# Kernel optimization log

Measured on AMD Instinct MI355X. Metric: run time of the kernel, lower is better.

The kernel has to match this reference:

```python
import jax, jax.numpy as jnp
import numpy as np


def _normal_distance(n1, n2):
    # Cosine-style normal distance: 1 - <n1, n2>. The original module stubs
    # this as 0; we use the canonical mesh-normal loss so the cdist+argmin+
    # gather chain is exercised end-to-end.
    return 1.0 - jnp.sum(n1 * n2, axis=-1)


def setup_inputs() -> dict:
    key = jax.random.key(0)
    k1, k2, k3, k4 = jax.random.split(key, 4)
    N, M = 8192, 32768
    pred_pts = jax.random.normal(k1, (1, N, 3), dtype=jnp.float32)
    pred_nrm = jax.random.normal(k2, (1, N, 3), dtype=jnp.float32)
    gt_pts = jax.random.normal(k3, (1, M, 3), dtype=jnp.float32)
    gt_nrm = jax.random.normal(k4, (1, M, 3), dtype=jnp.float32)
    # unit normals, as on a real mesh
    pred_nrm = pred_nrm / jnp.linalg.norm(pred_nrm, axis=-1, keepdims=True)
    gt_nrm = gt_nrm / jnp.linalg.norm(gt_nrm, axis=-1, keepdims=True)
    return {
        "predicted_points_batch": pred_pts,
        "predicted_normals_batch": pred_nrm,
        "gt_points_batch": gt_pts,
        "gt_normals_batch": gt_nrm,
    }


def reference(predicted_points_batch, predicted_normals_batch,
              gt_points_batch, gt_normals_batch):
    # Original forward returns inside the first loop iteration -> element 0 only.
    p = predicted_points_batch[0]    # [N,3]
    pn = predicted_normals_batch[0]  # [N,3]
    g = gt_points_batch[0]           # [M,3]
    gn = gt_normals_batch[0]         # [M,3]

    # Squared pairwise distances (monotone in true cdist; only argmin is used).
    # d2[i,j] = |p_i|^2 + |g_j|^2 - 2 p_i . g_j   -> one [N,M] intermediate.
    d2 = (jnp.sum(p * p, axis=1)[:, None]
          + jnp.sum(g * g, axis=1)[None, :]
          - 2.0 * (p @ g.T))                      # [N,M]

    gt_idx = jnp.argmin(d2, axis=1)    # nearest gt point per predicted point, [N]
    pr_idx = jnp.argmin(d2, axis=0)    # nearest predicted point per gt point, [M]

    nearest_gt_normals = gn[gt_idx]    # [N,3]
    nearest_pr_normals = pn[pr_idx]    # [M,3]

    dist1 = _normal_distance(pn, nearest_gt_normals)  # [N]
    dist2 = _normal_distance(gn, nearest_pr_normals)  # [M]
    return jnp.mean(dist1) + jnp.mean(dist2)
```

## Files before the change

kernel.cpp:

```cpp
#include <hip/hip_runtime.h>
#include <stdint.h>
#include <float.h>

#define BLK 256
#define IPT 8
#define OWNERS (BLK * IPT)
#define SLICE 128
#define SUB 64

typedef unsigned long long ull;

__device__ __forceinline__ unsigned int ford(float f) {
    int b = __float_as_int(f);
    return (b >= 0) ? ((unsigned)b ^ 0x80000000u) : ~(unsigned)b;
}
__device__ __forceinline__ float ford_inv(unsigned int u) {
    int b = (u & 0x80000000u) ? (int)(u ^ 0x80000000u) : (int)~u;
    return __int_as_float(b);
}

__global__ __launch_bounds__(BLK) void nn_min_dual(
    const float* __restrict__ p, const float* __restrict__ g,
    ull* __restrict__ rowmin, ull* __restrict__ colmin,
    int rowBlocks, int rowSlices, int colSlices)
{
    __shared__ float4 sb[SLICE];

    const float* A; const float* B; ull* outmin; int id, nSlices;
    if ((int)blockIdx.x < rowBlocks) {
        id = blockIdx.x;             A = p; B = g; outmin = rowmin; nSlices = rowSlices;
    } else {
        id = blockIdx.x - rowBlocks; A = g; B = p; outmin = colmin; nSlices = colSlices;
    }
    const int chunk = id / nSlices;
    const int slice = id - chunk * nSlices;
    const int s0 = slice * SLICE;

    if (threadIdx.x < SLICE) {
        int s = s0 + threadIdx.x;
        float bx = B[3 * s], by = B[3 * s + 1], bz = B[3 * s + 2];
        float w = fmaf(bz, bz, fmaf(by, by, bx * bx));
        sb[threadIdx.x] = make_float4(bx, by, bz, w);
    }

    const int o0 = chunk * OWNERS + threadIdx.x;
    float ax[IPT], ay[IPT], az[IPT], best[IPT];
    int base[IPT];
#pragma unroll
    for (int r = 0; r < IPT; ++r) {
        int o = o0 + r * BLK;
        ax[r] = -2.0f * A[3 * o];
        ay[r] = -2.0f * A[3 * o + 1];
        az[r] = -2.0f * A[3 * o + 2];
        best[r] = FLT_MAX;
        base[r] = s0;
    }
    __syncthreads();

    for (int st = 0; st < SLICE; st += SUB) {
        float prev[IPT];
#pragma unroll
        for (int r = 0; r < IPT; ++r) prev[r] = best[r];
#pragma unroll 4
        for (int k = st; k < st + SUB; ++k) {
            float4 q = sb[k];
#pragma unroll
            for (int r = 0; r < IPT; ++r) {
                float v = fmaf(ax[r], q.x, fmaf(ay[r], q.y, fmaf(az[r], q.z, q.w)));
                best[r] = fminf(best[r], v);
            }
        }
#pragma unroll
        for (int r = 0; r < IPT; ++r)
            if (best[r] < prev[r]) base[r] = s0 + st;
    }

#pragma unroll
    for (int r = 0; r < IPT; ++r) {
        ull packed = ((ull)ford(best[r]) << 32) | (unsigned)base[r];
        atomicMin(&outmin[o0 + r * BLK], packed);
    }
}

__global__ __launch_bounds__(BLK) void finalize_kernel(
    const ull* __restrict__ rowmin, const ull* __restrict__ colmin,
    const float* __restrict__ p, const float* __restrict__ g,
    const float* __restrict__ pn, const float* __restrict__ gn,
    float* __restrict__ out, int N, int M, float invN, float invM)
{
    int t = blockIdx.x * BLK + threadIdx.x;
    float c = 0.0f;
    if (t < N + M) {
        const float* A; const float* B; const float* An; const float* Bn;
        ull packed; int o; float inv;
        if (t < N) { o = t;     A = p; B = g; An = pn; Bn = gn; packed = rowmin[o]; inv = invN; }
        else       { o = t - N; A = g; B = p; An = gn; Bn = pn; packed = colmin[o]; inv = invM; }

        float ax = -2.0f * A[3 * o];
        float ay = -2.0f * A[3 * o + 1];
        float az = -2.0f * A[3 * o + 2];
        float bestf = ford_inv((unsigned int)(packed >> 32));
        int base = (int)(packed & 0xffffffffull);

        int idx = base;
        for (int j = 0; j < SUB; ++j) {
            int s = base + j;
            float bx = B[3 * s], by = B[3 * s + 1], bz = B[3 * s + 2];
            float w = fmaf(bz, bz, fmaf(by, by, bx * bx));
            float v = fmaf(ax, bx, fmaf(ay, by, fmaf(az, bz, w)));
            if (v == bestf) { idx = s; break; }
        }

        float d = An[3 * o] * Bn[3 * idx] + An[3 * o + 1] * Bn[3 * idx + 1]
                + An[3 * o + 2] * Bn[3 * idx + 2];
        c = (1.0f - d) * inv;
    }
#pragma unroll
    for (int off = 32; off > 0; off >>= 1) c += __shfl_down(c, off, 64);
    __shared__ float partial[BLK / 64];
    if ((threadIdx.x & 63) == 0) partial[threadIdx.x >> 6] = c;
    __syncthreads();
    if (threadIdx.x == 0) {
        float s = 0.0f;
#pragma unroll
        for (int w = 0; w < BLK / 64; ++w) s += partial[w];
        atomicAdd(out, s);
    }
}

extern "C" void kernel_launch(void* const* d_in, const int* in_sizes, int n_in,
                              void* d_out, int out_size, void* d_ws, size_t ws_size,
                              hipStream_t stream) {
    const float* p  = (const float*)d_in[0];
    const float* pn = (const float*)d_in[1];
    const float* g  = (const float*)d_in[2];
    const float* gn = (const float*)d_in[3];
    const int N = in_sizes[0] / 3;
    const int M = in_sizes[2] / 3;

    ull* rowmin = (ull*)d_ws;
    ull* colmin = rowmin + N;
    float* out = (float*)d_out;

    hipMemsetAsync(d_ws, 0xFF, (size_t)(N + M) * sizeof(ull), stream);
    hipMemsetAsync(d_out, 0, sizeof(float), stream);

    const int rowSlices = M / SLICE;
    const int colSlices = N / SLICE;
    const int rowBlocks = (N / OWNERS) * rowSlices;
    const int colBlocks = (M / OWNERS) * colSlices;
    nn_min_dual<<<rowBlocks + colBlocks, BLK, 0, stream>>>(
        p, g, rowmin, colmin, rowBlocks, rowSlices, colSlices);

    int tot = N + M;
    finalize_kernel<<<(tot + BLK - 1) / BLK, BLK, 0, stream>>>(
        rowmin, colmin, p, g, pn, gn, out, N, M, 1.0f / N, 1.0f / M);
}
```

Before: 114.4 us.

## Parallelize finalize rescan across wave lanes with ballot and pair-unroll distance loop

The finalize kernel now assigns each wavefront a group of owners and has the 64 lanes evaluate the 64 candidates of the winning sub-slice in parallel, using a ballot to find the first exact match instead of a serial per-thread scan with early break. The main distance loop processes two candidates per iteration and combines them with a min tree to shorten the dependency chain on the running minimum. The finalize change trades per-thread serial latency and divergence for more threads per owner and fewer blocks' worth of owners per wave.

Result: slower. 122.3 us (+6.9%).

```diff
diff --git a/kernel.cpp b/kernel.cpp
--- a/kernel.cpp
+++ b/kernel.cpp
@@ -7,6 +7,7 @@
 #define OWNERS (BLK * IPT)
 #define SLICE 128
 #define SUB 64
+#define FPW 16
 
 typedef unsigned long long ull;
 
@@ -61,13 +62,15 @@
         float prev[IPT];
 #pragma unroll
         for (int r = 0; r < IPT; ++r) prev[r] = best[r];
-#pragma unroll 4
-        for (int k = st; k < st + SUB; ++k) {
-            float4 q = sb[k];
+#pragma unroll 2
+        for (int k = st; k < st + SUB; k += 2) {
+            float4 q0 = sb[k];
+            float4 q1 = sb[k + 1];
 #pragma unroll
             for (int r = 0; r < IPT; ++r) {
-                float v = fmaf(ax[r], q.x, fmaf(ay[r], q.y, fmaf(az[r], q.z, q.w)));
-                best[r] = fminf(best[r], v);
+                float v0 = fmaf(ax[r], q0.x, fmaf(ay[r], q0.y, fmaf(az[r], q0.z, q0.w)));
+                float v1 = fmaf(ax[r], q1.x, fmaf(ay[r], q1.y, fmaf(az[r], q1.z, q1.w)));
+                best[r] = fminf(fminf(v0, v1), best[r]);
             }
         }
 #pragma unroll
@@ -88,9 +91,16 @@
     const float* __restrict__ pn, const float* __restrict__ gn,
     float* __restrict__ out, int N, int M, float invN, float invM)
 {
-    int t = blockIdx.x * BLK + threadIdx.x;
+    const int lane = threadIdx.x & 63;
+    const int waveInBlk = threadIdx.x >> 6;
+    const int wave = blockIdx.x * (BLK / 64) + waveInBlk;
+    const int t0 = wave * FPW;
     float c = 0.0f;
-    if (t < N + M) {
+
+#pragma unroll 1
+    for (int u = 0; u < FPW; ++u) {
+        int t = t0 + u;
+        if (t >= N + M) break;
         const float* A; const float* B; const float* An; const float* Bn;
         ull packed; int o; float inv;
         if (t < N) { o = t;     A = p; B = g; An = pn; Bn = gn; packed = rowmin[o]; inv = invN; }
@@ -102,23 +112,25 @@
         float bestf = ford_inv((unsigned int)(packed >> 32));
         int base = (int)(packed & 0xffffffffull);
 
-        int idx = base;
-        for (int j = 0; j < SUB; ++j) {
-            int s = base + j;
-            float bx = B[3 * s], by = B[3 * s + 1], bz = B[3 * s + 2];
-            float w = fmaf(bz, bz, fmaf(by, by, bx * bx));
-            float v = fmaf(ax, bx, fmaf(ay, by, fmaf(az, bz, w)));
-            if (v == bestf) { idx = s; break; }
+        int s = base + lane;
+        float bx = B[3 * s], by = B[3 * s + 1], bz = B[3 * s + 2];
+        float w = fmaf(bz, bz, fmaf(by, by, bx * bx));
+        float v = fmaf(ax, bx, fmaf(ay, by, fmaf(az, bz, w)));
+
+        ull m = __ballot(v == bestf);
+        int j = (m != 0ull) ? (__ffsll(m) - 1) : 0;
+        if (lane == j) {
+            int idx = base + j;
+            float d = An[3 * o] * Bn[3 * idx] + An[3 * o + 1] * Bn[3 * idx + 1]
+                    + An[3 * o + 2] * Bn[3 * idx + 2];
+            c += (1.0f - d) * inv;
         }
+    }
 
-        float d = An[3 * o] * Bn[3 * idx] + An[3 * o + 1] * Bn[3 * idx + 1]
-                + An[3 * o + 2] * Bn[3 * idx + 2];
-        c = (1.0f - d) * inv;
-    }
 #pragma unroll
     for (int off = 32; off > 0; off >>= 1) c += __shfl_down(c, off, 64);
     __shared__ float partial[BLK / 64];
-    if ((threadIdx.x & 63) == 0) partial[threadIdx.x >> 6] = c;
+    if (lane == 0) partial[waveInBlk] = c;
     __syncthreads();
     if (threadIdx.x == 0) {
         float s = 0.0f;
@@ -152,7 +164,9 @@
     nn_min_dual<<<rowBlocks + colBlocks, BLK, 0, stream>>>(
         p, g, rowmin, colmin, rowBlocks, rowSlices, colSlices);
 
-    int tot = N + M;
-    finalize_kernel<<<(tot + BLK - 1) / BLK, BLK, 0, stream>>>(
+    const int totOwners = N + M;
+    const int wavesNeeded = (totOwners + FPW - 1) / FPW;
+    const int finBlocks = (wavesNeeded + (BLK / 64) - 1) / (BLK / 64);
+    finalize_kernel<<<finBlocks, BLK, 0, stream>>>(
         rowmin, colmin, p, g, pn, gn, out, N, M, 1.0f / N, 1.0f / M);
 }
```

## Fuse memsets, NN search and finalize into one cooperative persistent kernel

Applied to the files above, without the earlier changes.

Replaces the two memsets and two kernel launches with a single cooperative kernel. It initializes the min buffers in-kernel, runs the dual nearest-neighbor search as a grid-stride loop over work units with grid.sync barriers, then does the finalize reduction. The inner loop is also restructured to process two points per iteration with a nested fmin, and the finalize search becomes branch-free. This removes launch and memset overhead, but adds the cost of grid-wide syncs and limits the grid to the number of blocks that can be resident at once.

Result: slower. 221.3 us (+93.4%).

```diff
diff --git a/kernel.cpp b/kernel.cpp
--- a/kernel.cpp
+++ b/kernel.cpp
@@ -1,6 +1,9 @@
 #include <hip/hip_runtime.h>
+#include <hip/hip_cooperative_groups.h>
 #include <stdint.h>
 #include <float.h>
+
+namespace cg = cooperative_groups;
 
 #define BLK 256
 #define IPT 8
@@ -19,102 +22,124 @@
     return __int_as_float(b);
 }
 
-__global__ __launch_bounds__(BLK) void nn_min_dual(
+__global__ __launch_bounds__(BLK) void fused(
     const float* __restrict__ p, const float* __restrict__ g,
-    ull* __restrict__ rowmin, ull* __restrict__ colmin,
-    int rowBlocks, int rowSlices, int colSlices)
+    const float* __restrict__ pn, const float* __restrict__ gn,
+    ull* __restrict__ mins, float* __restrict__ out, int N, int M)
 {
+    cg::grid_group grid = cg::this_grid();
+    const int gsize = gridDim.x * BLK;
+    const int gtid = blockIdx.x * BLK + threadIdx.x;
+    const int tot = N + M;
+
+    for (int t = gtid; t < tot; t += gsize)
+        __hip_atomic_store(&mins[t], ~0ull, __ATOMIC_RELAXED, __HIP_MEMORY_SCOPE_AGENT);
+    if (gtid == 0)
+        __hip_atomic_store(out, 0.0f, __ATOMIC_RELAXED, __HIP_MEMORY_SCOPE_AGENT);
+    grid.sync();
+
+    const int rowSlices = M / SLICE;
+    const int colSlices = N / SLICE;
+    const int rowWU = (N / OWNERS) * rowSlices;
+    const int colWU = (M / OWNERS) * colSlices;
+    const int totWU = rowWU + colWU;
+
     __shared__ float4 sb[SLICE];
 
-    const float* A; const float* B; ull* outmin; int id, nSlices;
-    if ((int)blockIdx.x < rowBlocks) {
-        id = blockIdx.x;             A = p; B = g; outmin = rowmin; nSlices = rowSlices;
-    } else {
-        id = blockIdx.x - rowBlocks; A = g; B = p; outmin = colmin; nSlices = colSlices;
-    }
-    const int chunk = id / nSlices;
-    const int slice = id - chunk * nSlices;
-    const int s0 = slice * SLICE;
+    for (int wu = blockIdx.x; wu < totWU; wu += gridDim.x) {
+        const float* A; const float* B; ull* outm; int id, nSlices;
+        if (wu < rowWU) { id = wu;         A = p; B = g; outm = mins;     nSlices = rowSlices; }
+        else            { id = wu - rowWU; A = g; B = p; outm = mins + N; nSlices = colSlices; }
+        const int chunk = id / nSlices;
+        const int slice = id - chunk * nSlices;
+        const int s0 = slice * SLICE;
 
-    if (threadIdx.x < SLICE) {
-        int s = s0 + threadIdx.x;
-        float bx = B[3 * s], by = B[3 * s + 1], bz = B[3 * s + 2];
-        float w = fmaf(bz, bz, fmaf(by, by, bx * bx));
-        sb[threadIdx.x] = make_float4(bx, by, bz, w);
+        __syncthreads();
+
+        if (threadIdx.x < SLICE) {
+            int s = s0 + threadIdx.x;
+            float bx = B[3 * s], by = B[3 * s + 1], bz = B[3 * s + 2];
+            float w = fmaf(bz, bz, fmaf(by, by, bx * bx));
+            sb[threadIdx.x] = make_float4(bx, by, bz, w);
+        }
+
+        const int o0 = chunk * OWNERS + threadIdx.x;
+        float ax[IPT], ay[IPT], az[IPT], best[IPT];
+        int base[IPT];
+#pragma unroll
+        for (int r = 0; r < IPT; ++r) {
+            int o = o0 + r * BLK;
+            ax[r] = -2.0f * A[3 * o];
+            ay[r] = -2.0f * A[3 * o + 1];
+            az[r] = -2.0f * A[3 * o + 2];
+            best[r] = FLT_MAX;
+            base[r] = s0;
+        }
+        __syncthreads();
+
+        for (int st = 0; st < SLICE; st += SUB) {
+            float prev[IPT];
+#pragma unroll
+            for (int r = 0; r < IPT; ++r) prev[r] = best[r];
+#pragma unroll 2
+            for (int k = st; k < st + SUB; k += 2) {
+                float4 q0 = sb[k];
+                float4 q1 = sb[k + 1];
+#pragma unroll
+                for (int r = 0; r < IPT; ++r) {
+                    float v0 = fmaf(ax[r], q0.x, fmaf(ay[r], q0.y, fmaf(az[r], q0.z, q0.w)));
+                    float v1 = fmaf(ax[r], q1.x, fmaf(ay[r], q1.y, fmaf(az[r], q1.z, q1.w)));
+                    best[r] = fminf(fminf(v0, v1), best[r]);
+                }
+            }
+#pragma unroll
+            for (int r = 0; r < IPT; ++r)
+                if (best[r] < prev[r]) base[r] = s0 + st;
+        }
+
+#pragma unroll
+        for (int r = 0; r < IPT; ++r) {
+            ull packed = ((ull)ford(best[r]) << 32) | (unsigned)base[r];
+            atomicMin(&outm[o0 + r * BLK], packed);
+        }
     }
 
-    const int o0 = chunk * OWNERS + threadIdx.x;
-    float ax[IPT], ay[IPT], az[IPT], best[IPT];
-    int base[IPT];
-#pragma unroll
-    for (int r = 0; r < IPT; ++r) {
-        int o = o0 + r * BLK;
-        ax[r] = -2.0f * A[3 * o];
-        ay[r] = -2.0f * A[3 * o + 1];
-        az[r] = -2.0f * A[3 * o + 2];
-        best[r] = FLT_MAX;
-        base[r] = s0;
-    }
-    __syncthreads();
+    grid.sync();
 
-    for (int st = 0; st < SLICE; st += SUB) {
-        float prev[IPT];
-#pragma unroll
-        for (int r = 0; r < IPT; ++r) prev[r] = best[r];
-#pragma unroll 4
-        for (int k = st; k < st + SUB; ++k) {
-            float4 q = sb[k];
-#pragma unroll
-            for (int r = 0; r < IPT; ++r) {
-                float v = fmaf(ax[r], q.x, fmaf(ay[r], q.y, fmaf(az[r], q.z, q.w)));
-                best[r] = fminf(best[r], v);
-            }
-        }
-#pragma unroll
-        for (int r = 0; r < IPT; ++r)
-            if (best[r] < prev[r]) base[r] = s0 + st;
-    }
+    const float invN = 1.0f / (float)N;
+    const float invM = 1.0f / (float)M;
+    float c = 0.0f;
 
-#pragma unroll
-    for (int r = 0; r < IPT; ++r) {
-        ull packed = ((ull)ford(best[r]) << 32) | (unsigned)base[r];
-        atomicMin(&outmin[o0 + r * BLK], packed);
-    }
-}
+    for (int t = gtid; t < tot; t += gsize) {
+        const float* A; const float* B; const float* An; const float* Bn;
+        int o; float inv;
+        if (t < N) { o = t;     A = p; B = g; An = pn; Bn = gn; inv = invN; }
+        else       { o = t - N; A = g; B = p; An = gn; Bn = pn; inv = invM; }
 
-__global__ __launch_bounds__(BLK) void finalize_kernel(
-    const ull* __restrict__ rowmin, const ull* __restrict__ colmin,
-    const float* __restrict__ p, const float* __restrict__ g,
-    const float* __restrict__ pn, const float* __restrict__ gn,
-    float* __restrict__ out, int N, int M, float invN, float invM)
-{
-    int t = blockIdx.x * BLK + threadIdx.x;
-    float c = 0.0f;
-    if (t < N + M) {
-        const float* A; const float* B; const float* An; const float* Bn;
-        ull packed; int o; float inv;
-        if (t < N) { o = t;     A = p; B = g; An = pn; Bn = gn; packed = rowmin[o]; inv = invN; }
-        else       { o = t - N; A = g; B = p; An = gn; Bn = pn; packed = colmin[o]; inv = invM; }
-
+        ull packed = __hip_atomic_load(&mins[t], __ATOMIC_RELAXED, __HIP_MEMORY_SCOPE_AGENT);
         float ax = -2.0f * A[3 * o];
         float ay = -2.0f * A[3 * o + 1];
         float az = -2.0f * A[3 * o + 2];
         float bestf = ford_inv((unsigned int)(packed >> 32));
-        int base = (int)(packed & 0xffffffffull);
+        int b0 = (int)(packed & 0xffffffffull);
 
-        int idx = base;
+        int idx = 0x7fffffff;
+#pragma unroll 4
         for (int j = 0; j < SUB; ++j) {
-            int s = base + j;
+            int s = b0 + j;
             float bx = B[3 * s], by = B[3 * s + 1], bz = B[3 * s + 2];
             float w = fmaf(bz, bz, fmaf(by, by, bx * bx));
             float v = fmaf(ax, bx, fmaf(ay, by, fmaf(az, bz, w)));
-            if (v == bestf) { idx = s; break; }
+            int cand = (v == bestf) ? s : 0x7fffffff;
+            idx = (cand < idx) ? cand : idx;
         }
+        if (idx == 0x7fffffff) idx = b0;
 
         float d = An[3 * o] * Bn[3 * idx] + An[3 * o + 1] * Bn[3 * idx + 1]
                 + An[3 * o + 2] * Bn[3 * idx + 2];
-        c = (1.0f - d) * inv;
+        c += (1.0f - d) * inv;
     }
+
 #pragma unroll
     for (int off = 32; off > 0; off >>= 1) c += __shfl_down(c, off, 64);
     __shared__ float partial[BLK / 64];
@@ -124,7 +149,7 @@
         float s = 0.0f;
 #pragma unroll
         for (int w = 0; w < BLK / 64; ++w) s += partial[w];
-        atomicAdd(out, s);
+        if (s != 0.0f) atomicAdd(out, s);
     }
 }
 
@@ -138,21 +163,21 @@
     const int N = in_sizes[0] / 3;
     const int M = in_sizes[2] / 3;
 
-    ull* rowmin = (ull*)d_ws;
-    ull* colmin = rowmin + N;
+    ull* mins = (ull*)d_ws;
     float* out = (float*)d_out;
 
-    hipMemsetAsync(d_ws, 0xFF, (size_t)(N + M) * sizeof(ull), stream);
-    hipMemsetAsync(d_out, 0, sizeof(float), stream);
+    static int gridBlocks = 0;
+    if (gridBlocks == 0) {
+        int occ = 0, numCU = 0;
+        hipOccupancyMaxActiveBlocksPerMultiprocessor(&occ, (const void*)fused, BLK, 0);
+        hipDeviceGetAttribute(&numCU, hipDeviceAttributeMultiprocessorCount, 0);
+        int mb = occ * numCU;
+        if (mb < 64) mb = 64;
+        gridBlocks = mb > 2048 ? 2048 : mb;
+    }
 
-    const int rowSlices = M / SLICE;
-    const int colSlices = N / SLICE;
-    const int rowBlocks = (N / OWNERS) * rowSlices;
-    const int colBlocks = (M / OWNERS) * colSlices;
-    nn_min_dual<<<rowBlocks + colBlocks, BLK, 0, stream>>>(
-        p, g, rowmin, colmin, rowBlocks, rowSlices, colSlices);
-
-    int tot = N + M;
-    finalize_kernel<<<(tot + BLK - 1) / BLK, BLK, 0, stream>>>(
-        rowmin, colmin, p, g, pn, gn, out, N, M, 1.0f / N, 1.0f / M);
+    void* args[] = { (void*)&p, (void*)&g, (void*)&pn, (void*)&gn,
+                     (void*)&mins, (void*)&out, (void*)&N, (void*)&M };
+    hipLaunchCooperativeKernel((const void*)fused, dim3(gridBlocks), dim3(BLK),
+                               args, 0, stream);
 }
```

## Replace atomic min reduction with per-slice partial buffers and separate reduce kernel

Applied to the files above, without the earlier changes.

Instead of every block issuing 64-bit atomicMin to a shared row/column minimum array, each block now writes its per-slice packed minimum into a dedicated workspace slot. A new reduce kernel scans those slots to pick the global minimum before the normal-distance finalize. This removes the two memsets because the output is zeroed inside the first kernel. Slices grow to 256 points and the inner loop processes two candidates per step. The trade is roughly 16 MB of extra workspace traffic against the atomic contention it replaces. The old path is kept as a fallback when the workspace is too small or the sizes don't fit the tiling.

New measurement: 122.4 us. +7.0%, slower.

```diff
diff --git a/kernel.cpp b/kernel.cpp
--- a/kernel.cpp
+++ b/kernel.cpp
@@ -5,7 +5,8 @@
 #define BLK 256
 #define IPT 8
 #define OWNERS (BLK * IPT)
-#define SLICE 128
+#define SLICE2 256
+#define SLICE1 128
 #define SUB 64
 
 typedef unsigned long long ull;
@@ -19,24 +20,27 @@
     return __int_as_float(b);
 }
 
-__global__ __launch_bounds__(BLK) void nn_min_dual(
-    const float* __restrict__ p, const float* __restrict__ g,
-    ull* __restrict__ rowmin, ull* __restrict__ colmin,
-    int rowBlocks, int rowSlices, int colSlices)
-{
-    __shared__ float4 sb[SLICE];
-
-    const float* A; const float* B; ull* outmin; int id, nSlices;
+__global__ __launch_bounds__(BLK) void nn_slices(
+    const float* __restrict__ p, const float* __restrict__ g,
+    ull* __restrict__ wsR, ull* __restrict__ wsC,
+    float* __restrict__ out, int N, int M)
+{
+    __shared__ float4 sb[SLICE2];
+
+    if (blockIdx.x == 0 && threadIdx.x == 0) *out = 0.0f;
+
+    const int rowBlocks = (N / OWNERS) * (M / SLICE2);
+    const float* A; const float* B; ull* ws; int id, nSlices, NO;
     if ((int)blockIdx.x < rowBlocks) {
-        id = blockIdx.x;             A = p; B = g; outmin = rowmin; nSlices = rowSlices;
+        id = blockIdx.x;             A = p; B = g; ws = wsR; nSlices = M / SLICE2; NO = N;
     } else {
-        id = blockIdx.x - rowBlocks; A = g; B = p; outmin = colmin; nSlices = colSlices;
+        id = blockIdx.x - rowBlocks; A = g; B = p; ws = wsC; nSlices = N / SLICE2; NO = M;
     }
     const int chunk = id / nSlices;
-    const int slice = id - chunk * nSlices;
-    const int s0 = slice * SLICE;
-
-    if (threadIdx.x < SLICE) {
+    const int j = id - chunk * nSlices;
+    const int s0 = j * SLICE2;
+
+    {
         int s = s0 + threadIdx.x;
         float bx = B[3 * s], by = B[3 * s + 1], bz = B[3 * s + 2];
         float w = fmaf(bz, bz, fmaf(by, by, bx * bx));
@@ -57,17 +61,19 @@
     }
     __syncthreads();
 
-    for (int st = 0; st < SLICE; st += SUB) {
+    for (int st = 0; st < SLICE2; st += SUB) {
         float prev[IPT];
 #pragma unroll
         for (int r = 0; r < IPT; ++r) prev[r] = best[r];
-#pragma unroll 4
-        for (int k = st; k < st + SUB; ++k) {
-            float4 q = sb[k];
+#pragma unroll 2
+        for (int k = st; k < st + SUB; k += 2) {
+            float4 q0 = sb[k];
+            float4 q1 = sb[k + 1];
 #pragma unroll
             for (int r = 0; r < IPT; ++r) {
-                float v = fmaf(ax[r], q.x, fmaf(ay[r], q.y, fmaf(az[r], q.z, q.w)));
-                best[r] = fminf(best[r], v);
+                float v0 = fmaf(ax[r], q0.x, fmaf(ay[r], q0.y, fmaf(az[r], q0.z, q0.w)));
+                float v1 = fmaf(ax[r], q1.x, fmaf(ay[r], q1.y, fmaf(az[r], q1.z, q1.w)));
+                best[r] = fminf(fminf(v0, v1), best[r]);
             }
         }
 #pragma unroll
@@ -75,6 +81,117 @@
             if (best[r] < prev[r]) base[r] = s0 + st;
     }
 
+    ull* dst = ws + (size_t)j * NO;
+#pragma unroll
+    for (int r = 0; r < IPT; ++r)
+        dst[o0 + r * BLK] = ((ull)ford(best[r]) << 32) | (unsigned)base[r];
+}
+
+__global__ __launch_bounds__(BLK) void reduce_fin(
+    const ull* __restrict__ wsR, const ull* __restrict__ wsC,
+    const float* __restrict__ p, const float* __restrict__ g,
+    const float* __restrict__ pn, const float* __restrict__ gn,
+    float* __restrict__ out, int N, int M, float invN, float invM)
+{
+    int t = blockIdx.x * BLK + threadIdx.x;
+    float c = 0.0f;
+    if (t < N + M) {
+        const float* A; const float* B; const float* An; const float* Bn;
+        const ull* ws; int o, K, NO; float inv;
+        if (t < N) { o = t;     A = p; B = g; An = pn; Bn = gn; ws = wsR; K = M / SLICE2; NO = N; inv = invN; }
+        else       { o = t - N; A = g; B = p; An = gn; Bn = pn; ws = wsC; K = N / SLICE2; NO = M; inv = invM; }
+
+        ull bestp = ws[o];
+#pragma unroll 4
+        for (int jj = 1; jj < K; ++jj) {
+            ull v2 = ws[(size_t)jj * NO + o];
+            bestp = (v2 < bestp) ? v2 : bestp;
+        }
+
+        float ax = -2.0f * A[3 * o];
+        float ay = -2.0f * A[3 * o + 1];
+        float az = -2.0f * A[3 * o + 2];
+        float bestf = ford_inv((unsigned int)(bestp >> 32));
+        int b0 = (int)(bestp & 0xffffffffull);
+
+        int idx = 0x7fffffff;
+#pragma unroll 4
+        for (int jj = 0; jj < SUB; ++jj) {
+            int s = b0 + jj;
+            float bx = B[3 * s], by = B[3 * s + 1], bz = B[3 * s + 2];
+            float w = fmaf(bz, bz, fmaf(by, by, bx * bx));
+            float v = fmaf(ax, bx, fmaf(ay, by, fmaf(az, bz, w)));
+            int cand = (v == bestf) ? s : 0x7fffffff;
+            idx = (cand < idx) ? cand : idx;
+        }
+        if (idx == 0x7fffffff) idx = b0;
+
+        float d = An[3 * o] * Bn[3 * idx] + An[3 * o + 1] * Bn[3 * idx + 1]
+                + An[3 * o + 2] * Bn[3 * idx + 2];
+        c = (1.0f - d) * inv;
+    }
+#pragma unroll
+    for (int off = 32; off > 0; off >>= 1) c += __shfl_down(c, off, 64);
+    __shared__ float partial[BLK / 64];
+    if ((threadIdx.x & 63) == 0) partial[threadIdx.x >> 6] = c;
+    __syncthreads();
+    if (threadIdx.x == 0) {
+        float s = 0.0f;
+#pragma unroll
+        for (int w = 0; w < BLK / 64; ++w) s += partial[w];
+        atomicAdd(out, s);
+    }
+}
+
+__global__ __launch_bounds__(BLK) void nn_min_dual(
+    const float* __restrict__ p, const float* __restrict__ g,
+    ull* __restrict__ rowmin, ull* __restrict__ colmin,
+    int rowBlocks, int rowSlices, int colSlices)
+{
+    __shared__ float4 sb[SLICE1];
+    const float* A; const float* B; ull* outmin; int id, nSlices;
+    if ((int)blockIdx.x < rowBlocks) {
+        id = blockIdx.x;             A = p; B = g; outmin = rowmin; nSlices = rowSlices;
+    } else {
+        id = blockIdx.x - rowBlocks; A = g; B = p; outmin = colmin; nSlices = colSlices;
+    }
+    const int chunk = id / nSlices;
+    const int slice = id - chunk * nSlices;
+    const int s0 = slice * SLICE1;
+    if (threadIdx.x < SLICE1) {
+        int s = s0 + threadIdx.x;
+        float bx = B[3 * s], by = B[3 * s + 1], bz = B[3 * s + 2];
+        float w = fmaf(bz, bz, fmaf(by, by, bx * bx));
+        sb[threadIdx.x] = make_float4(bx, by, bz, w);
+    }
+    const int o0 = chunk * OWNERS + threadIdx.x;
+    float ax[IPT], ay[IPT], az[IPT], best[IPT];
+    int base[IPT];
+#pragma unroll
+    for (int r = 0; r < IPT; ++r) {
+        int o = o0 + r * BLK;
+        ax[r] = -2.0f * A[3 * o]; ay[r] = -2.0f * A[3 * o + 1]; az[r] = -2.0f * A[3 * o + 2];
+        best[r] = FLT_MAX; base[r] = s0;
+    }
+    __syncthreads();
+    for (int st = 0; st < SLICE1; st += SUB) {
+        float prev[IPT];
+#pragma unroll
+        for (int r = 0; r < IPT; ++r) prev[r] = best[r];
+#pragma unroll 2
+        for (int k = st; k < st + SUB; k += 2) {
+            float4 q0 = sb[k]; float4 q1 = sb[k + 1];
+#pragma unroll
+            for (int r = 0; r < IPT; ++r) {
+                float v0 = fmaf(ax[r], q0.x, fmaf(ay[r], q0.y, fmaf(az[r], q0.z, q0.w)));
+                float v1 = fmaf(ax[r], q1.x, fmaf(ay[r], q1.y, fmaf(az[r], q1.z, q1.w)));
+                best[r] = fminf(fminf(v0, v1), best[r]);
+            }
+        }
+#pragma unroll
+        for (int r = 0; r < IPT; ++r)
+            if (best[r] < prev[r]) base[r] = s0 + st;
+    }
 #pragma unroll
     for (int r = 0; r < IPT; ++r) {
         ull packed = ((ull)ford(best[r]) << 32) | (unsigned)base[r];
@@ -82,7 +199,7 @@
     }
 }
 
-__global__ __launch_bounds__(BLK) void finalize_kernel(
+__global__ __launch_bounds__(BLK) void finalize_legacy(
     const ull* __restrict__ rowmin, const ull* __restrict__ colmin,
     const float* __restrict__ p, const float* __restrict__ g,
     const float* __restrict__ pn, const float* __restrict__ gn,
@@ -95,22 +212,20 @@
         ull packed; int o; float inv;
         if (t < N) { o = t;     A = p; B = g; An = pn; Bn = gn; packed = rowmin[o]; inv = invN; }
         else       { o = t - N; A = g; B = p; An = gn; Bn = pn; packed = colmin[o]; inv = invM; }
-
-        float ax = -2.0f * A[3 * o];
-        float ay = -2.0f * A[3 * o + 1];
-        float az = -2.0f * A[3 * o + 2];
+        float ax = -2.0f * A[3 * o], ay = -2.0f * A[3 * o + 1], az = -2.0f * A[3 * o + 2];
         float bestf = ford_inv((unsigned int)(packed >> 32));
-        int base = (int)(packed & 0xffffffffull);
-
-        int idx = base;
-        for (int j = 0; j < SUB; ++j) {
-            int s = base + j;
+        int b0 = (int)(packed & 0xffffffffull);
+        int idx = 0x7fffffff;
+#pragma unroll 4
+        for (int jj = 0; jj < SUB; ++jj) {
+            int s = b0 + jj;
             float bx = B[3 * s], by = B[3 * s + 1], bz = B[3 * s + 2];
             float w = fmaf(bz, bz, fmaf(by, by, bx * bx));
             float v = fmaf(ax, bx, fmaf(ay, by, fmaf(az, bz, w)));
-            if (v == bestf) { idx = s; break; }
-        }
-
+            int cand = (v == bestf) ? s : 0x7fffffff;
+            idx = (cand < idx) ? cand : idx;
+        }
+        if (idx == 0x7fffffff) idx = b0;
         float d = An[3 * o] * Bn[3 * idx] + An[3 * o + 1] * Bn[3 * idx + 1]
                 + An[3 * o + 2] * Bn[3 * idx + 2];
         c = (1.0f - d) * inv;
@@ -137,22 +252,34 @@
     const float* gn = (const float*)d_in[3];
     const int N = in_sizes[0] / 3;
     const int M = in_sizes[2] / 3;
-
-    ull* rowmin = (ull*)d_ws;
-    ull* colmin = rowmin + N;
     float* out = (float*)d_out;
 
-    hipMemsetAsync(d_ws, 0xFF, (size_t)(N + M) * sizeof(ull), stream);
-    hipMemsetAsync(d_out, 0, sizeof(float), stream);
-
-    const int rowSlices = M / SLICE;
-    const int colSlices = N / SLICE;
-    const int rowBlocks = (N / OWNERS) * rowSlices;
-    const int colBlocks = (M / OWNERS) * colSlices;
-    nn_min_dual<<<rowBlocks + colBlocks, BLK, 0, stream>>>(
-        p, g, rowmin, colmin, rowBlocks, rowSlices, colSlices);
-
-    int tot = N + M;
-    finalize_kernel<<<(tot + BLK - 1) / BLK, BLK, 0, stream>>>(
-        rowmin, colmin, p, g, pn, gn, out, N, M, 1.0f / N, 1.0f / M);
-}
+    const size_t needR = (size_t)(M / SLICE2) * N * sizeof(ull);
+    const size_t needC = (size_t)(N / SLICE2) * M * sizeof(ull);
+    const bool geomOK = (N % OWNERS) == 0 && (M % OWNERS) == 0 &&
+                        (N % SLICE2) == 0 && (M % SLICE2) == 0 &&
+                        ((N + M) % BLK) == 0;
+
+    if (geomOK && ws_size >= needR + needC) {
+        ull* wsR = (ull*)d_ws;
+        ull* wsC = wsR + (size_t)(M / SLICE2) * N;
+        const int blocks = (N / OWNERS) * (M / SLICE2) + (M / OWNERS) * (N / SLICE2);
+        nn_slices<<<blocks, BLK, 0, stream>>>(p, g, wsR, wsC, out, N, M);
+        reduce_fin<<<(N + M) / BLK, BLK, 0, stream>>>(
+            wsR, wsC, p, g, pn, gn, out, N, M, 1.0f / N, 1.0f / M);
+    } else {
+        ull* rowmin = (ull*)d_ws;
+        ull* colmin = rowmin + N;
+        hipMemsetAsync(d_ws, 0xFF, (size_t)(N + M) * sizeof(ull), stream);
+        hipMemsetAsync(d_out, 0, sizeof(float), stream);
+        const int rowSlices = M / SLICE1;
+        const int colSlices = N / SLICE1;
+        const int rowBlocks = (N / OWNERS) * rowSlices;
+        const int colBlocks = (M / OWNERS) * colSlices;
+        nn_min_dual<<<rowBlocks + colBlocks, BLK, 0, stream>>>(
+            p, g, rowmin, colmin, rowBlocks, rowSlices, colSlices);
+        int tot = N + M;
+        finalize_legacy<<<(tot + BLK - 1) / BLK, BLK, 0, stream>>>(
+            rowmin, colmin, p, g, pn, gn, out, N, M, 1.0f / N, 1.0f / M);
+    }
+}
```
